# Optimization experiments

Measured on AMD Instinct MI355X. Metric: run time of the kernel, lower is better.

## Reference

```python
import jax, jax.numpy as jnp
import numpy as np

B, L, DIM = 16, 4096, 512
N_FFT, HOP, WIN = 1024, 256, 1024
PAD = (WIN - HOP) // 2  # 'same' padding trim
OUT_DIM = N_FFT + 2


def hann_window(win):
    n = jnp.arange(win, dtype=jnp.float32)
    return 0.5 - 0.5 * jnp.cos(2.0 * jnp.pi * n / win)


def setup_inputs() -> dict:
    key = jax.random.key(0)
    k1, k2 = jax.random.split(key)
    x = jax.random.normal(k1, (B, L, DIM), dtype=jnp.float32)
    W = jax.random.normal(k2, (OUT_DIM, DIM), dtype=jnp.float32) * 0.02
    b = jnp.zeros((OUT_DIM,), dtype=jnp.float32)
    return {"x": x, "W": W, "b": b}


def _istft(S):
    # S: (B, N_FFT//2+1, T) complex rfft spectrum
    T = S.shape[-1]
    frames = jnp.fft.irfft(S, n=N_FFT, axis=1)
    window = hann_window(WIN)
    frames = frames * window[None, :, None]
    out_len = (T - 1) * HOP + WIN
    idx = jnp.arange(T)[:, None] * HOP + jnp.arange(WIN)[None, :]
    fr = frames.transpose(0, 2, 1)
    y = jnp.zeros((fr.shape[0], out_len), fr.dtype).at[:, idx].add(fr)
    env = jnp.zeros((out_len,), fr.dtype).at[idx].add(
        jnp.broadcast_to(window * window, idx.shape))
    y = y[:, PAD:out_len - PAD]
    env = env[PAD:out_len - PAD]
    return y / env


def reference(x, W, b):
    # Linear projection: (B, L, DIM) -> (B, L, N_FFT+2)
    h = jnp.einsum('bld,od->blo', x, W) + b
    h = h.transpose(0, 2, 1)                              # (B, N_FFT+2, L)
    mag, p = jnp.split(h, 2, axis=1)                      # each (B, N_FFT//2+1, L)
    mag = jnp.minimum(jnp.exp(mag), 100.0)                # exp + clip(max=100)
    S = mag * jax.lax.complex(jnp.cos(p), jnp.sin(p))
    return _istft(S)                                      # (B, L*HOP)
```

## Files before the change

kernel.cpp:

```cpp
#include <hip/hip_runtime.h>
#include <hip/hip_bf16.h>
#include <math.h>

#define BATCH   16
#define TFRM    4096
#define DIM     512
#define NFFT    1024
#define HOP     256
#define PADC    384
#define MROWS   (BATCH*TFRM)
#define OUTLEN  1048576
#define ESTR    520
#define TWO_PI_OVER_N 0.006135923151542565f
#define INV_TWO_PI    0.15915494309189535f

typedef __bf16 bf16x8 __attribute__((ext_vector_type(8)));
typedef float  f32x4  __attribute__((ext_vector_type(4)));

__device__ __forceinline__ ushort f2bf(float f) {
  union { float f; unsigned u; } v; v.f = f;
  unsigned u = v.u;
  unsigned r = (u + 0x7FFFu + ((u >> 16) & 1u)) >> 16;
  return (ushort)r;
}
__device__ __forceinline__ float bf2f(ushort h) {
  union { unsigned u; float f; } v; v.u = ((unsigned)h) << 16;
  return v.f;
}
__device__ __forceinline__ float fast_sin(float x) { return __builtin_amdgcn_sinf(x * INV_TWO_PI); }
__device__ __forceinline__ float fast_cos(float x) { return __builtin_amdgcn_cosf(x * INV_TWO_PI); }
__device__ __forceinline__ float fast_exp(float x) { return __builtin_amdgcn_exp2f(x * 1.4426950408889634f); }

__global__ void k_prep_x(const float* __restrict__ x, const float* __restrict__ W,
                         const float* __restrict__ bias,
                         ushort* __restrict__ xbf, float* __restrict__ s512) {
  const int row  = blockIdx.x * 4 + (threadIdx.x >> 6);
  const int lane = threadIdx.x & 63;
  const float* xr = x + (size_t)row * DIM + lane * 8;
  float4 v0 = *(const float4*)xr;
  float4 v1 = *(const float4*)(xr + 4);
  ushort4 u0, u1;
  u0.x = f2bf(v0.x); u0.y = f2bf(v0.y); u0.z = f2bf(v0.z); u0.w = f2bf(v0.w);
  u1.x = f2bf(v1.x); u1.y = f2bf(v1.y); u1.z = f2bf(v1.z); u1.w = f2bf(v1.w);
  ushort* xo = xbf + (size_t)row * DIM + lane * 8;
  *(ushort4*)xo = u0;
  *(ushort4*)(xo + 4) = u1;
  const float* w0 = W + 512 * DIM + lane * 8;
  const float* w1 = W + 1025 * DIM + lane * 8;
  float4 a0 = *(const float4*)w0, a1 = *(const float4*)(w0 + 4);
  float4 b0 = *(const float4*)w1, b1 = *(const float4*)(w1 + 4);
  float sm = v0.x*a0.x + v0.y*a0.y + v0.z*a0.z + v0.w*a0.w
           + v1.x*a1.x + v1.y*a1.y + v1.z*a1.z + v1.w*a1.w;
  float sp = v0.x*b0.x + v0.y*b0.y + v0.z*b0.z + v0.w*b0.w
           + v1.x*b1.x + v1.y*b1.y + v1.z*b1.z + v1.w*b1.w;
#pragma unroll
  for (int off = 32; off; off >>= 1) {
    sm += __shfl_down(sm, off);
    sp += __shfl_down(sp, off);
  }
  if (lane == 0) {
    float mag = fminf(fast_exp(sm + bias[512]), 100.0f);
    s512[row] = mag * fast_cos(sp + bias[1025]) * (1.0f / 1024.0f);
  }
}

__global__ void k_prep_w(const float* __restrict__ W, ushort* __restrict__ o) {
  int i = blockIdx.x * 256 + threadIdx.x;
  int r = i >> 9;
  int c = i & 511;
  int orig = (r >> 1) + (r & 1) * 513;
  o[i] = f2bf(W[orig * DIM + c]);
}

__global__ void k_basis(ushort* __restrict__ basE, ushort* __restrict__ basO) {
  int r = blockIdx.x;
  int n = r + 1;
  for (int k = threadIdx.x; k < 512; k += 256) {
    float e, o;
    if (k == 0) { e = 1.0f / 1024.0f; o = 0.0f; }
    else {
      int ph = (k * n) & 1023;
      float ang = (float)ph * TWO_PI_OVER_N;
      e = 2.0f * cosf(ang) * (1.0f / 1024.0f);
      o = 2.0f * sinf(ang) * (1.0f / 1024.0f);
    }
    basE[r * 512 + k] = f2bf(e);
    basO[r * 512 + k] = f2bf(o);
  }
}

template<int EPI>
__global__ __launch_bounds__(256) void k_gemm(const ushort* A, const ushort* A2, int lda,
                                              const ushort* Bt, const ushort* Bt2, int ldb,
                                              ushort* C, ushort* C2, int ldc,
                                              int nbn, int NK, int nsplit,
                                              const float* __restrict__ bias,
                                              const float* __restrict__ s512) {
  __shared__ __align__(16) ushort lds[3][2][128 * 32];
  const int tid  = threadIdx.x;
  const int cpx  = gridDim.x >> 3;
  int bid  = (blockIdx.x & 7) * cpx + (blockIdx.x >> 3);
  bool second = false;
  if (nsplit > 0 && bid >= nsplit) { second = true; A = A2; Bt = Bt2; C = C2; bid -= nsplit; }
  const int bm   = bid / nbn;
  const int bn   = bid - bm * nbn;
  const int lane = tid & 63;
  const int wv   = tid >> 6;
  const int wr   = (wv >> 1) * 64;
  const int wc   = (wv & 1) * 64;
  const int lr   = lane & 15;
  const int gx   = ((lane >> 4) ^ ((lane >> 1) & 3)) << 3;

  f32x4 acc[4][4] = {};

  const int swz = ((tid & 3) ^ ((tid >> 3) & 3)) << 3;
  auto stage = [&](const ushort* __restrict__ g, int ld, int row0, int k0, ushort* l) {
#pragma unroll
    for (int p = 0; p < 2; ++p) {
      int i = tid + p * 256;
      const ushort* gp = g + (size_t)(row0 + (i >> 2)) * ld + k0 + swz;
      ushort* lp = l + ((i >> 6) << 9);
      __builtin_amdgcn_global_load_lds(
          (const __attribute__((address_space(1))) void*)gp,
          (__attribute__((address_space(3))) void*)lp, 16, 0, 0);
    }
  };

  stage(A,  lda, bm * 128, 0,  &lds[0][0][0]);
  stage(Bt, ldb, bn * 128, 0,  &lds[0][1][0]);
  stage(A,  lda, bm * 128, 32, &lds[1][0][0]);
  stage(Bt, ldb, bn * 128, 32, &lds[1][1][0]);
  asm volatile("s_waitcnt vmcnt(4)" ::: "memory");
  __syncthreads();

  int sl = 0;
  for (int t = 0; t < NK; ++t) {
    if (t + 2 < NK) {
      const int psl = (sl >= 1) ? sl - 1 : 2;
      stage(A,  lda, bm * 128, (t + 2) << 5, &lds[psl][0][0]);
      stage(Bt, ldb, bn * 128, (t + 2) << 5, &lds[psl][1][0]);
    }
    const ushort* lA = &lds[sl][0][0];
    const ushort* lB = &lds[sl][1][0];
    bf16x8 aF[4], bF[4];
#pragma unroll
    for (int m = 0; m < 4; ++m)
      aF[m] = *(const bf16x8*)(lA + (wr + m * 16 + lr) * 32 + gx);
#pragma unroll
    for (int n = 0; n < 4; ++n)
      bF[n] = *(const bf16x8*)(lB + (wc + n * 16 + lr) * 32 + gx);
#pragma unroll
    for (int m = 0; m < 4; ++m)
#pragma unroll
      for (int n = 0; n < 4; ++n)
        acc[m][n] = __builtin_amdgcn_mfma_f32_16x16x32_bf16(aF[m], bF[n], acc[m][n], 0, 0, 0);
    if (t + 2 < NK)      asm volatile("s_waitcnt vmcnt(4)" ::: "memory");
    else if (t + 2 == NK) asm volatile("s_waitcnt vmcnt(0)" ::: "memory");
    if (t + 1 < NK) __syncthreads();
    sl = (sl >= 2) ? 0 : sl + 1;
  }

  const int r0 = bm * 128 + wr + ((lane >> 4) << 2);
  const int c0 = bn * 128 + wc + lr;
#pragma unroll
  for (int m = 0; m < 4; ++m) {
    if constexpr (EPI == 0) {
      float4 sv4 = {0.f, 0.f, 0.f, 0.f};
      if (!second) sv4 = *(const float4*)(s512 + r0 + m * 16);
#pragma unroll
      for (int j = 0; j < 4; ++j) {
        size_t ro = (size_t)(r0 + m * 16 + j) * ldc;
        float sv = ((const float*)&sv4)[j];
#pragma unroll
        for (int n = 0; n < 4; ++n) {
          int c = c0 + n * 16;
          float par = second ? 0.0f : ((c & 1) ? sv : -sv);
          C[ro + c + 1] = f2bf(acc[m][n][j] + par);
        }
      }
    } else {
#pragma unroll
      for (int n = 0; n < 4; ++n) {
        const int col = c0 + n * 16;
        const int kk  = col >> 1;
        const bool isPhase = (col & 1);
        const float bs = bias[isPhase ? 513 + kk : kk];
        ushort* dst = (isPhase ? C2 : C);
#pragma unroll
        for (int j = 0; j < 4; ++j) {
          float v = acc[m][n][j] + bs;
          float pv = __shfl_xor(v, 1);
          float hm = isPhase ? pv : v;
          float hp = isPhase ? v : pv;
          float mag = fminf(fast_exp(hm), 100.0f);
          float outv = isPhase ? mag * fast_sin(hp) : mag * fast_cos(hp);
          dst[(size_t)(r0 + m * 16 + j) * ldc + kk] = f2bf(outv);
        }
      }
    }
  }
}

__global__ void k_oa(const ushort* __restrict__ E, const ushort* __restrict__ O,
                     float* __restrict__ out) {
  int u = blockIdx.x * 256 + threadIdx.x;
  int b  = u >> 18;
  int g  = u & 262143;
  int s  = (g << 2) + PADC;
  int t0 = s >> 8;
  int nb = s & 255;
  float acc[4] = {0.f, 0.f, 0.f, 0.f};
  bool interior = (t0 >= 3) && (t0 < TFRM);
  float env[4];
#pragma unroll
  for (int j = 0; j < 4; ++j) env[j] = interior ? 1.5f : 0.0f;
#pragma unroll
  for (int q = 0; q < 4; ++q) {
    int t = t0 - q;
    if (t < 0 || t >= TFRM) continue;
    int n = nb + (q << 8);
    size_t base = ((size_t)(b << 12) + t) * ESTR;
    float w[4];
#pragma unroll
    for (int j = 0; j < 4; ++j) {
      w[j] = 0.5f - 0.5f * __builtin_amdgcn_cosf((float)(n + j) * (1.0f / 1024.0f));
      if (!interior) env[j] += w[j] * w[j];
    }
    float d[4];
    if (n + 3 <= 512) {
      ushort4 e = *(const ushort4*)(E + base + n);
      ushort4 o = *(const ushort4*)(O + base + n);
      d[0] = bf2f(e.x) - bf2f(o.x); d[1] = bf2f(e.y) - bf2f(o.y);
      d[2] = bf2f(e.z) - bf2f(o.z); d[3] = bf2f(e.w) - bf2f(o.w);
    } else if (n >= 516) {
      int m2 = 1024 - n;
      ushort4 e0 = *(const ushort4*)(E + base + m2);
      ushort4 e1 = *(const ushort4*)(E + base + m2 - 4);
      ushort4 o0 = *(const ushort4*)(O + base + m2);
      ushort4 o1 = *(const ushort4*)(O + base + m2 - 4);
      d[0] = bf2f(e0.x) + bf2f(o0.x); d[1] = bf2f(e1.w) + bf2f(o1.w);
      d[2] = bf2f(e1.z) + bf2f(o1.z); d[3] = bf2f(e1.y) + bf2f(o1.y);
    } else {
      d[0] = bf2f(E[base + 512]) - bf2f(O[base + 512]);
      d[1] = bf2f(E[base + 511]) + bf2f(O[base + 511]);
      d[2] = bf2f(E[base + 510]) + bf2f(O[base + 510]);
      d[3] = bf2f(E[base + 509]) + bf2f(O[base + 509]);
    }
#pragma unroll
    for (int j = 0; j < 4; ++j) acc[j] += w[j] * d[j];
  }
  float4 o4;
  o4.x = acc[0] / env[0]; o4.y = acc[1] / env[1];
  o4.z = acc[2] / env[2]; o4.w = acc[3] / env[3];
  *(float4*)(out + (size_t)u * 4) = o4;
}

extern "C" void kernel_launch(void* const* d_in, const int* in_sizes, int n_in,
                              void* d_out, int out_size, void* d_ws, size_t ws_size,
                              hipStream_t stream) {
  const float* x    = (const float*)d_in[0];
  const float* W    = (const float*)d_in[1];
  const float* bias = (const float*)d_in[2];
  float* out = (float*)d_out;
  char* ws = (char*)d_ws;

  ushort* xbf  = (ushort*)(ws + 0);
  ushort* Epp  = (ushort*)(ws + 0);
  ushort* h_a  = (ushort*)(ws + 68157440);
  ushort* h_b  = (ushort*)(ws + 135266304);
  ushort* Obuf = (ushort*)(ws + 202375168);
  ushort* Wp   = (ushort*)(ws + 270532608);
  ushort* basE = (ushort*)(ws + 271581184);
  ushort* basO = (ushort*)(ws + 272105472);
  float*  s512 = (float*) (ws + 272629760);

  k_prep_x<<<MROWS / 4, 256, 0, stream>>>(x, W, bias, xbf, s512);
  k_prep_w<<<(1024 * 512) / 256, 256, 0, stream>>>(W, Wp);
  k_basis<<<512, 256, 0, stream>>>(basE, basO);

  k_gemm<1><<<(MROWS / 128) * 8, 256, 0, stream>>>(
      xbf, nullptr, DIM, Wp, nullptr, DIM, h_a, h_b, 512, 8, 16, 0, bias, nullptr);

  k_gemm<0><<<2 * (MROWS / 128) * 4, 256, 0, stream>>>(
      h_a, h_b, 512, basE, basO, 512, Epp, Obuf, ESTR, 4, 16, (MROWS / 128) * 4,
      nullptr, s512);

  k_oa<<<(BATCH * OUTLEN) / 1024, 256, 0, stream>>>(Epp, Obuf, out);
}
```

Baseline: 310.8 us.

## Stage GEMM epilogues through LDS for coalesced 16-byte stores, use 512-stride spectra

Both GEMM epilogues now write their accumulator tiles into shared memory and then copy them out as contiguous 16-byte vector stores, replacing scattered 2-byte global writes. The second GEMM's output row stride drops from 520 to 512 with a shifted column mapping. The overlap-add kernel's index math and mirrored loads are adjusted to match, with one extra aligned load per frame. The lane-pair swap in the first epilogue uses a DPP intrinsic instead of a shuffle. This adds LDS traffic and barriers, and the rewritten boundary indexing risks off-by-one errors.

```diff
diff --git a/kernel.cpp b/kernel.cpp
--- a/kernel.cpp
+++ b/kernel.cpp
@@ -10,7 +10,6 @@
 #define PADC    384
 #define MROWS   (BATCH*TFRM)
 #define OUTLEN  1048576
-#define ESTR    520
 #define TWO_PI_OVER_N 0.006135923151542565f
 #define INV_TWO_PI    0.15915494309189535f
 
@@ -30,6 +29,10 @@
 __device__ __forceinline__ float fast_sin(float x) { return __builtin_amdgcn_sinf(x * INV_TWO_PI); }
 __device__ __forceinline__ float fast_cos(float x) { return __builtin_amdgcn_cosf(x * INV_TWO_PI); }
 __device__ __forceinline__ float fast_exp(float x) { return __builtin_amdgcn_exp2f(x * 1.4426950408889634f); }
+__device__ __forceinline__ float dpp_xor1(float v) {
+  return __int_as_float(__builtin_amdgcn_update_dpp(
+      __float_as_int(v), __float_as_int(v), 0xB1, 0xF, 0xF, false));
+}
 
 __global__ void k_prep_x(const float* __restrict__ x, const float* __restrict__ W,
                          const float* __restrict__ bias,
@@ -160,43 +163,71 @@
     sl = (sl >= 2) ? 0 : sl + 1;
   }
 
-  const int r0 = bm * 128 + wr + ((lane >> 4) << 2);
-  const int c0 = bn * 128 + wc + lr;
-#pragma unroll
-  for (int m = 0; m < 4; ++m) {
-    if constexpr (EPI == 0) {
+  const int rl = wr + ((lane >> 4) << 2);
+  const int r0 = bm * 128 + rl;
+  ushort* epi = &lds[0][0][0];
+  __syncthreads();
+
+  if constexpr (EPI == 0) {
+#pragma unroll
+    for (int m = 0; m < 4; ++m) {
       float4 sv4 = {0.f, 0.f, 0.f, 0.f};
       if (!second) sv4 = *(const float4*)(s512 + r0 + m * 16);
 #pragma unroll
       for (int j = 0; j < 4; ++j) {
-        size_t ro = (size_t)(r0 + m * 16 + j) * ldc;
         float sv = ((const float*)&sv4)[j];
+        int row = rl + m * 16 + j;
 #pragma unroll
         for (int n = 0; n < 4; ++n) {
-          int c = c0 + n * 16;
+          int c = wc + n * 16 + lr;
           float par = second ? 0.0f : ((c & 1) ? sv : -sv);
-          C[ro + c + 1] = f2bf(acc[m][n][j] + par);
+          epi[row * 144 + c] = f2bf(acc[m][n][j] + par);
         }
       }
-    } else {
+    }
+    __syncthreads();
+#pragma unroll
+    for (int i = 0; i < 8; ++i) {
+      int row = (tid >> 4) + i * 16;
+      int co  = (tid & 15) << 3;
+      bf16x8 v = *(const bf16x8*)(epi + row * 144 + co);
+      *(bf16x8*)(C + (size_t)(bm * 128 + row) * ldc + bn * 128 + co) = v;
+    }
+  } else {
+    ushort* tA = epi;
+    ushort* tB = epi + 128 * 80;
+#pragma unroll
+    for (int m = 0; m < 4; ++m) {
 #pragma unroll
       for (int n = 0; n < 4; ++n) {
-        const int col = c0 + n * 16;
-        const int kk  = col >> 1;
-        const bool isPhase = (col & 1);
+        const int cl  = wc + n * 16 + lr;
+        const int kk  = (bn * 128 + cl) >> 1;
+        const bool isPhase = (cl & 1);
         const float bs = bias[isPhase ? 513 + kk : kk];
-        ushort* dst = (isPhase ? C2 : C);
+        ushort* dst = (isPhase ? tB : tA);
+        const int kkl = cl >> 1;
 #pragma unroll
         for (int j = 0; j < 4; ++j) {
           float v = acc[m][n][j] + bs;
-          float pv = __shfl_xor(v, 1);
+          float pv = dpp_xor1(v);
           float hm = isPhase ? pv : v;
           float hp = isPhase ? v : pv;
           float mag = fminf(fast_exp(hm), 100.0f);
           float outv = isPhase ? mag * fast_sin(hp) : mag * fast_cos(hp);
-          dst[(size_t)(r0 + m * 16 + j) * ldc + kk] = f2bf(outv);
+          dst[(rl + m * 16 + j) * 80 + kkl] = f2bf(outv);
         }
       }
+    }
+    __syncthreads();
+#pragma unroll
+    for (int i = 0; i < 4; ++i) {
+      int row = (tid >> 3) + i * 32;
+      int co  = (tid & 7) << 3;
+      size_t go = (size_t)(bm * 128 + row) * ldc + bn * 64 + co;
+      bf16x8 va = *(const bf16x8*)(tA + row * 80 + co);
+      *(bf16x8*)(C + go) = va;
+      bf16x8 vb = *(const bf16x8*)(tB + row * 80 + co);
+      *(bf16x8*)(C2 + go) = vb;
     }
   }
 }
@@ -219,7 +250,7 @@
     int t = t0 - q;
     if (t < 0 || t >= TFRM) continue;
     int n = nb + (q << 8);
-    size_t base = ((size_t)(b << 12) + t) * ESTR;
+    size_t base = ((size_t)(b << 12) + t) << 9;
     float w[4];
 #pragma unroll
     for (int j = 0; j < 4; ++j) {
@@ -227,24 +258,31 @@
       if (!interior) env[j] += w[j] * w[j];
     }
     float d[4];
-    if (n + 3 <= 512) {
-      ushort4 e = *(const ushort4*)(E + base + n);
-      ushort4 o = *(const ushort4*)(O + base + n);
-      d[0] = bf2f(e.x) - bf2f(o.x); d[1] = bf2f(e.y) - bf2f(o.y);
-      d[2] = bf2f(e.z) - bf2f(o.z); d[3] = bf2f(e.w) - bf2f(o.w);
-    } else if (n >= 516) {
-      int m2 = 1024 - n;
-      ushort4 e0 = *(const ushort4*)(E + base + m2);
-      ushort4 e1 = *(const ushort4*)(E + base + m2 - 4);
-      ushort4 o0 = *(const ushort4*)(O + base + m2);
-      ushort4 o1 = *(const ushort4*)(O + base + m2 - 4);
-      d[0] = bf2f(e0.x) + bf2f(o0.x); d[1] = bf2f(e1.w) + bf2f(o1.w);
-      d[2] = bf2f(e1.z) + bf2f(o1.z); d[3] = bf2f(e1.y) + bf2f(o1.y);
+    if (n <= 508) {
+      ushort4 e1 = *(const ushort4*)(E + base + n);
+      ushort4 o1 = *(const ushort4*)(O + base + n);
+      if (n >= 4) {
+        ushort4 e0 = *(const ushort4*)(E + base + n - 4);
+        ushort4 o0 = *(const ushort4*)(O + base + n - 4);
+        d[0] = bf2f(e0.w) - bf2f(o0.w);
+      } else d[0] = 0.0f;
+      d[1] = bf2f(e1.x) - bf2f(o1.x);
+      d[2] = bf2f(e1.y) - bf2f(o1.y);
+      d[3] = bf2f(e1.z) - bf2f(o1.z);
+    } else if (n == 512) {
+      ushort4 e = *(const ushort4*)(E + base + 508);
+      ushort4 o = *(const ushort4*)(O + base + 508);
+      d[0] = bf2f(e.w) - bf2f(o.w);
+      d[1] = bf2f(e.z) + bf2f(o.z);
+      d[2] = bf2f(e.y) + bf2f(o.y);
+      d[3] = bf2f(e.x) + bf2f(o.x);
     } else {
-      d[0] = bf2f(E[base + 512]) - bf2f(O[base + 512]);
-      d[1] = bf2f(E[base + 511]) + bf2f(O[base + 511]);
-      d[2] = bf2f(E[base + 510]) + bf2f(O[base + 510]);
-      d[3] = bf2f(E[base + 509]) + bf2f(O[base + 509]);
+      ushort4 e = *(const ushort4*)(E + base + 1020 - n);
+      ushort4 o = *(const ushort4*)(O + base + 1020 - n);
+      d[0] = bf2f(e.w) + bf2f(o.w);
+      d[1] = bf2f(e.z) + bf2f(o.z);
+      d[2] = bf2f(e.y) + bf2f(o.y);
+      d[3] = bf2f(e.x) + bf2f(o.x);
     }
 #pragma unroll
     for (int j = 0; j < 4; ++j) acc[j] += w[j] * d[j];
@@ -266,13 +304,13 @@
 
   ushort* xbf  = (ushort*)(ws + 0);
   ushort* Epp  = (ushort*)(ws + 0);
-  ushort* h_a  = (ushort*)(ws + 68157440);
-  ushort* h_b  = (ushort*)(ws + 135266304);
-  ushort* Obuf = (ushort*)(ws + 202375168);
-  ushort* Wp   = (ushort*)(ws + 270532608);
-  ushort* basE = (ushort*)(ws + 271581184);
-  ushort* basO = (ushort*)(ws + 272105472);
-  float*  s512 = (float*) (ws + 272629760);
+  ushort* h_a  = (ushort*)(ws + 67108864);
+  ushort* h_b  = (ushort*)(ws + 134217728);
+  ushort* Obuf = (ushort*)(ws + 201326592);
+  ushort* Wp   = (ushort*)(ws + 268435456);
+  ushort* basE = (ushort*)(ws + 269484032);
+  ushort* basO = (ushort*)(ws + 270008320);
+  float*  s512 = (float*) (ws + 270532608);
 
   k_prep_x<<<MROWS / 4, 256, 0, stream>>>(x, W, bias, xbf, s512);
   k_prep_w<<<(1024 * 512) / 256, 256, 0, stream>>>(W, Wp);
@@ -282,7 +320,7 @@
       xbf, nullptr, DIM, Wp, nullptr, DIM, h_a, h_b, 512, 8, 16, 0, bias, nullptr);
 
   k_gemm<0><<<2 * (MROWS / 128) * 4, 256, 0, stream>>>(
-      h_a, h_b, 512, basE, basO, 512, Epp, Obuf, ESTR, 4, 16, (MROWS / 128) * 4,
+      h_a, h_b, 512, basE, basO, 512, Epp, Obuf, 512, 4, 16, (MROWS / 128) * 4,
       nullptr, s512);
 
   k_oa<<<(BATCH * OUTLEN) / 1024, 256, 0, stream>>>(Epp, Obuf, out);
```

Result: faster. 294.1 us (-5.4%).
